# Kernel optimization log

Hardware: AMD Instinct MI355X
Metric: run time of the kernel (lower is better)

Reference implementation:

```python
import jax, jax.numpy as jnp
import numpy as np


def lstm_cell(x, h, c, Wih, Whh, bih, bhh):
    # PyTorch LSTMCell: gates ordered (i, f, g, o)
    gates = x @ Wih.T + h @ Whh.T + bih + bhh
    i, f, g, o = jnp.split(gates, 4, axis=-1)
    c_new = jax.nn.sigmoid(f) * c + jax.nn.sigmoid(i) * jnp.tanh(g)
    h_new = jax.nn.sigmoid(o) * jnp.tanh(c_new)
    return h_new, c_new


def setup_inputs() -> dict:
    key = jax.random.key(0)
    B, S, I, H = 64, 1024, 300, 512
    ks = jax.random.split(key, 9)
    s0 = 1.0 / np.sqrt(H)  # PyTorch LSTMCell default init range

    def u(k, shape):
        return jax.random.uniform(k, shape, jnp.float32, -s0, s0)

    return {
        "input": jax.random.normal(ks[0], (B, S, I), jnp.float32),
        "Wih0": u(ks[1], (4 * H, I)),
        "Whh0": u(ks[2], (4 * H, H)),
        "bih0": u(ks[3], (4 * H,)),
        "bhh0": u(ks[4], (4 * H,)),
        "Wih1": u(ks[5], (4 * H, H)),
        "Whh1": u(ks[6], (4 * H, H)),
        "bih1": u(ks[7], (4 * H,)),
        "bhh1": u(ks[8], (4 * H,)),
    }


def reference(input, Wih0, Whh0, bih0, bhh0, Wih1, Whh1, bih1, bhh1):
    B, S, I = input.shape
    H = Whh0.shape[1]
    h0 = c0 = h1 = c1 = jnp.zeros((B, H), input.dtype)  # self.h0/self.c0 zeros

    def step(carry, x_t):
        h0, c0, h1, c1 = carry
        h0, c0 = lstm_cell(x_t, h0, c0, Wih0, Whh0, bih0, bhh0)
        h1, c1 = lstm_cell(h0, h1, c1, Wih1, Whh1, bih1, bhh1)
        return (h0, c0, h1, c1), (h1, c1)

    xs = jnp.swapaxes(input, 0, 1)  # [S, B, I]
    (h0, c0, h1, c1), (out, c_out) = jax.lax.scan(step, (h0, c0, h1, c1), xs)
    out = jnp.swapaxes(out, 0, 1)      # [B, S, H]
    c_out = jnp.swapaxes(c_out, 0, 1)  # [B, S, H]
    return ((out, c_out), (h1, c1))
```

## Files before the change

### kernel.cpp

```cpp
#include <hip/hip_runtime.h>

#define NB 64
#define NS 1024
#define NI 300
#define NH 512
#define L0WG 32
#define NWG 64

typedef _Float16 f16;
typedef f16 half8 __attribute__((ext_vector_type(8)));
typedef float floatx4 __attribute__((ext_vector_type(4)));
typedef unsigned long long u64;
typedef unsigned u32;
typedef u32 u32x4 __attribute__((ext_vector_type(4)));

__device__ __attribute__((aligned(64))) f16 g_X[NS][NB][320];
__device__ __attribute__((aligned(64))) f16 g_H0[4][NB][NH];
__device__ __attribute__((aligned(64))) f16 g_H1[4][NB][NH];
__device__ u32 g_f0[NS][32];
__device__ u32 g_f1[NS][32];
__device__ u32 g_fI[NWG];

__device__ __forceinline__ float sigm(float x){ return 1.f/(1.f+__expf(-x)); }
__device__ __forceinline__ float tanh_(float x){ return 1.f - 2.f/(__expf(2.f*x)+1.f); }

__device__ __forceinline__ u32 ldc(const u32* p){
  return __hip_atomic_load(p, __ATOMIC_RELAXED, __HIP_MEMORY_SCOPE_AGENT);
}
__device__ __forceinline__ void sig(u32* p, u32 v){
  __hip_atomic_store(p, v, __ATOMIC_RELAXED, __HIP_MEMORY_SCOPE_AGENT);
}

#define STR_(x) #x
#define STR(x) STR_(x)
#define CLOAD16(dst, base, OFF) \
  asm volatile("global_load_dwordx4 %0, %1, off offset:" STR(OFF) " sc1" \
               : "=v"(dst) : "v"(base))
#define CLOADN16(dst, base, OFF) \
  asm volatile("global_load_dwordx4 %0, %1, off offset:" STR(OFF) \
               : "=v"(dst) : "v"(base))
#define CSTORE16(base, val) \
  asm volatile("global_store_dwordx4 %0, %1, off sc1" :: "v"(base), "v"(val))
#define VWAIT(N) do { asm volatile("s_waitcnt vmcnt(" STR(N) ")" ::: "memory"); \
  __builtin_amdgcn_sched_barrier(0); } while(0)
#define MFMA(acc, a, b) acc = __builtin_amdgcn_mfma_f32_16x16x32_f16(a, b, acc, 0, 0, 0)

#define HLOADS(arr, p) do { \
  CLOAD16(arr[0],  p, 0);   CLOAD16(arr[1],  p, 64);  \
  CLOAD16(arr[2],  p, 128); CLOAD16(arr[3],  p, 192); \
  CLOAD16(arr[4],  p, 256); CLOAD16(arr[5],  p, 320); \
  CLOAD16(arr[6],  p, 384); CLOAD16(arr[7],  p, 448); \
  CLOAD16(arr[8],  p, 512); CLOAD16(arr[9],  p, 576); \
  CLOAD16(arr[10], p, 640); CLOAD16(arr[11], p, 704); \
  CLOAD16(arr[12], p, 768); CLOAD16(arr[13], p, 832); \
  CLOAD16(arr[14], p, 896); CLOAD16(arr[15], p, 960); } while(0)

__device__ __forceinline__ void pollA(const u32* pa, const u32* pb, u32 E, int lane){
  const u32* p = nullptr;
  if (lane < 8) p = pa + lane * 4;
  else if (lane < 16 && pb) p = pb + (lane - 8) * 4;
  for (;;){
    bool ok = true;
    if (p){
      u32x4 v;
      asm volatile("global_load_dwordx4 %0, %1, off sc1" : "=v"(v) : "v"(p));
      asm volatile("s_waitcnt vmcnt(0)" ::: "memory");
      ok = ((int)(v[0]-E) >= 0) & ((int)(v[1]-E) >= 0) &
           ((int)(v[2]-E) >= 0) & ((int)(v[3]-E) >= 0);
    }
    if (__all(ok)) return;
    __builtin_amdgcn_s_sleep(1);
  }
}

__global__ void __launch_bounds__(256, 1) lstm_persist(
    const float* __restrict__ xin,
    const float* __restrict__ Wih0, const float* __restrict__ Whh0,
    const float* __restrict__ bih0, const float* __restrict__ bhh0,
    const float* __restrict__ Wih1, const float* __restrict__ Whh1,
    const float* __restrict__ bih1, const float* __restrict__ bhh1,
    float* __restrict__ out)
{
  __shared__ f16   WB[96 * 640];
  __shared__ f16   sh_h[4][16][24];
  __shared__ float sh_o[4][2][16][20];

  const int wg = blockIdx.x, tid = threadIdx.x;
  const int wv = tid >> 6, lane = tid & 63, n15 = lane & 15, g4 = lane >> 4;
  const int kb = g4 * 8;
  const int mrow = wv * 16 + n15;
  const bool isL1 = (wg >= L0WG);
  const int wgi = isL1 ? wg - L0WG : wg;
  const int j0 = wgi * 16;
  const int bb = n15 * 40 + kb;

  const u32 E = ldc(&g_f1[NS - 1][0]) + 1;

  const int jc = j0 + n15;
  float bi, bf, bg, bo;
  float creg[4] = {0.f, 0.f, 0.f, 0.f};

  if (!isL1) {
    bi = bih0[jc] + bhh0[jc];          bf = bih0[NH + jc] + bhh0[NH + jc];
    bg = bih0[2*NH + jc] + bhh0[2*NH + jc]; bo = bih0[3*NH + jc] + bhh0[3*NH + jc];

    {
      const int b = tid >> 2, q = tid & 3;
      for (int r = 0; r < 32; ++r) {
        const int t = wgi * 32 + r;
        const float* xr = xin + ((size_t)b * NS + t) * NI;
        u64* dst = (u64*)&g_X[t][b][0];
        #pragma unroll
        for (int e = 0; e < 20; ++e) {
          const int idx = q * 20 + e;
          u64 v = 0;
          if (idx < 75) {
            const float4 f = *(const float4*)(xr + (idx << 2));
            union { f16 h[4]; u64 u; } pk;
            pk.h[0]=(f16)f.x; pk.h[1]=(f16)f.y; pk.h[2]=(f16)f.z; pk.h[3]=(f16)f.w;
            v = pk.u;
          }
          dst[idx] = v;
        }
      }
    }
    if (tid < 64) {
      half8 z = {};
      CSTORE16(&g_H0[3][tid][j0], z);
      CSTORE16(&g_H0[3][tid][j0 + 8], z);
    }
    for (int idx = tid; idx < 52 * 16; idx += 256) {
      const int u = idx >> 4, n = idx & 15;
      const int gl = 2 + (u >= 26);
      const int ch = (u >= 26) ? u - 26 : u;
      const int grow = gl * NH + j0 + n;
      f16* dst = &WB[u * 640 + n * 40];
      for (int k = 0; k < 32; ++k) {
        const int kk = ch * 32 + k;
        float v;
        if (kk < NI) v = Wih0[(size_t)grow * NI + kk];
        else if (kk < 320) v = 0.f;
        else v = Whh0[(size_t)grow * NH + (kk - 320)];
        dst[k] = (f16)v;
      }
    }
    half8 w_i[26], w_f[26];
    {
      const int gi = j0 + n15, gf = NH + j0 + n15;
      #pragma unroll
      for (int ch = 0; ch < 26; ++ch) {
        union { f16 h[8]; half8 v; } pi, pf;
        #pragma unroll
        for (int jj = 0; jj < 8; ++jj) {
          const int kk = ch * 32 + kb + jj;
          pi.h[jj] = (f16)((kk < NI) ? Wih0[(size_t)gi * NI + kk]
                     : (kk < 320) ? 0.f : Whh0[(size_t)gi * NH + (kk - 320)]);
          pf.h[jj] = (f16)((kk < NI) ? Wih0[(size_t)gf * NI + kk]
                     : (kk < 320) ? 0.f : Whh0[(size_t)gf * NH + (kk - 320)]);
        }
        w_i[ch] = pi.v; w_f[ch] = pf.v;
      }
    }
    VWAIT(0);
    __threadfence();
    __syncthreads();
    if (tid == 0) sig(&g_fI[wg], E);
    if (wv == 0) {
      pollA(&g_fI[0], nullptr, E, lane);
      pollA(&g_fI[32], nullptr, E, lane);
    }
    __syncthreads();

    half8 xa[10];
    {
      const f16* xp = &g_X[0][mrow][0] + kb;
      CLOADN16(xa[0], xp, 0);   CLOADN16(xa[1], xp, 64);
      CLOADN16(xa[2], xp, 128); CLOADN16(xa[3], xp, 192);
      CLOADN16(xa[4], xp, 256); CLOADN16(xa[5], xp, 320);
      CLOADN16(xa[6], xp, 384); CLOADN16(xa[7], xp, 448);
      CLOADN16(xa[8], xp, 512); CLOADN16(xa[9], xp, 576);
    }

    for (int t = 0; t < NS; ++t) {
      if (t > 0) {
        if (wv == 0) pollA(&g_f0[t-1][0], (t >= 4) ? &g_f1[t-4][0] : nullptr, E, lane);
        __syncthreads();
      }
      const f16* hp = &g_H0[(t + 3) & 3][mrow][0] + kb;
      half8 ha[16];
      HLOADS(ha, hp);
      floatx4 ai = {0,0,0,0}, af = {0,0,0,0}, ag = {0,0,0,0}, ao = {0,0,0,0};
      VWAIT(16);
      #pragma unroll
      for (int ci = 0; ci < 10; ++ci) {
        const half8 a = xa[ci];
        MFMA(ai, a, w_i[ci]); MFMA(af, a, w_f[ci]);
        MFMA(ag, a, *(const half8*)&WB[ci * 640 + bb]);
        MFMA(ao, a, *(const half8*)&WB[(26 + ci) * 640 + bb]);
      }
      VWAIT(8);
      #pragma unroll
      for (int ci = 10; ci < 18; ++ci) {
        const half8 a = ha[ci - 10];
        MFMA(ai, a, w_i[ci]); MFMA(af, a, w_f[ci]);
        MFMA(ag, a, *(const half8*)&WB[ci * 640 + bb]);
        MFMA(ao, a, *(const half8*)&WB[(26 + ci) * 640 + bb]);
      }
      VWAIT(0);
      #pragma unroll
      for (int ci = 18; ci < 26; ++ci) {
        const half8 a = ha[ci - 10];
        MFMA(ai, a, w_i[ci]); MFMA(af, a, w_f[ci]);
        MFMA(ag, a, *(const half8*)&WB[ci * 640 + bb]);
        MFMA(ao, a, *(const half8*)&WB[(26 + ci) * 640 + bb]);
      }
      #pragma unroll
      for (int r = 0; r < 4; ++r) {
        const float vi = ai[r] + bi, vf = af[r] + bf;
        const float vg = ag[r] + bg, vo = ao[r] + bo;
        const float cn = sigm(vf) * creg[r] + sigm(vi) * tanh_(vg);
        const float hn = sigm(vo) * tanh_(cn);
        creg[r] = cn;
        sh_h[wv][g4 * 4 + r][n15] = (f16)hn;
      }
      asm volatile("s_waitcnt lgkmcnt(0)" ::: "memory");
      __builtin_amdgcn_sched_barrier(0);
      if (lane < 32) {
        const half8 hv = *(const half8*)&sh_h[wv][lane >> 1][(lane & 1) * 8];
        CSTORE16(&g_H0[t & 3][wv * 16 + (lane >> 1)][j0 + (lane & 1) * 8], hv);
      }
      VWAIT(0);
      __syncthreads();
      if (tid == 0) sig(&g_f0[t][wgi], E);
      if (t + 1 < NS) {
        const f16* xp = &g_X[t + 1][mrow][0] + kb;
        CLOADN16(xa[0], xp, 0);   CLOADN16(xa[1], xp, 64);
        CLOADN16(xa[2], xp, 128); CLOADN16(xa[3], xp, 192);
        CLOADN16(xa[4], xp, 256); CLOADN16(xa[5], xp, 320);
        CLOADN16(xa[6], xp, 384); CLOADN16(xa[7], xp, 448);
        CLOADN16(xa[8], xp, 512); CLOADN16(xa[9], xp, 576);
      }
    }

  } else {
    bi = bih1[jc] + bhh1[jc];          bf = bih1[NH + jc] + bhh1[NH + jc];
    bg = bih1[2*NH + jc] + bhh1[2*NH + jc]; bo = bih1[3*NH + jc] + bhh1[3*NH + jc];

    if (tid < 64) {
      half8 z = {};
      CSTORE16(&g_H1[3][tid][j0], z);
      CSTORE16(&g_H1[3][tid][j0 + 8], z);
    }
    for (int idx = tid; idx < 96 * 16; idx += 256) {
      const int u = idx >> 4, n = idx & 15;
      const int gl = 1 + (u >> 5);
      const int ch = u & 31;
      const int grow = gl * NH + j0 + n;
      f16* dst = &WB[u * 640 + n * 40];
      for (int k = 0; k < 32; ++k) {
        const int kk = ch * 32 + k;
        const float v = (kk < NH) ? Wih1[(size_t)grow * NH + kk]
                                  : Whh1[(size_t)grow * NH + (kk - NH)];
        dst[k] = (f16)v;
      }
    }
    half8 w_i1[32];
    {
      const int gi = j0 + n15;
      #pragma unroll
      for (int ch = 0; ch < 32; ++ch) {
        union { f16 h[8]; half8 v; } pk;
        #pragma unroll
        for (int jj = 0; jj < 8; ++jj) {
          const int kk = ch * 32 + kb + jj;
          pk.h[jj] = (f16)((kk < NH) ? Wih1[(size_t)gi * NH + kk]
                                     : Whh1[(size_t)gi * NH + (kk - NH)]);
        }
        w_i1[ch] = pk.v;
      }
    }
    VWAIT(0);
    __syncthreads();
    if (tid == 0) sig(&g_fI[wg], E);
    if (wv == 0) {
      pollA(&g_fI[0], nullptr, E, lane);
      pollA(&g_fI[32], nullptr, E, lane);
    }
    __syncthreads();

    for (int t = 0; t < NS; ++t) {
      if (wv == 0) pollA(&g_f0[t][0], (t >= 1) ? &g_f1[t-1][0] : nullptr, E, lane);
      __syncthreads();
      const f16* p0 = &g_H0[t & 3][mrow][0] + kb;
      const f16* p1 = &g_H1[(t + 3) & 3][mrow][0] + kb;
      half8 ha[16], hb[16];
      HLOADS(ha, p0);
      HLOADS(hb, p1);
      floatx4 ai = {0,0,0,0}, af = {0,0,0,0}, ag = {0,0,0,0}, ao = {0,0,0,0};
      VWAIT(24);
      #pragma unroll
      for (int ci = 0; ci < 8; ++ci) {
        const half8 a = ha[ci];
        MFMA(ai, a, w_i1[ci]);
        MFMA(af, a, *(const half8*)&WB[ci * 640 + bb]);
        MFMA(ag, a, *(const half8*)&WB[(32 + ci) * 640 + bb]);
        MFMA(ao, a, *(const half8*)&WB[(64 + ci) * 640 + bb]);
      }
      VWAIT(16);
      #pragma unroll
      for (int ci = 8; ci < 16; ++ci) {
        const half8 a = ha[ci];
        MFMA(ai, a, w_i1[ci]);
        MFMA(af, a, *(const half8*)&WB[ci * 640 + bb]);
        MFMA(ag, a, *(const half8*)&WB[(32 + ci) * 640 + bb]);
        MFMA(ao, a, *(const half8*)&WB[(64 + ci) * 640 + bb]);
      }
      VWAIT(8);
      #pragma unroll
      for (int ci = 16; ci < 24; ++ci) {
        const half8 a = hb[ci - 16];
        MFMA(ai, a, w_i1[ci]);
        MFMA(af, a, *(const half8*)&WB[ci * 640 + bb]);
        MFMA(ag, a, *(const half8*)&WB[(32 + ci) * 640 + bb]);
        MFMA(ao, a, *(const half8*)&WB[(64 + ci) * 640 + bb]);
      }
      VWAIT(0);
      #pragma unroll
      for (int ci = 24; ci < 32; ++ci) {
        const half8 a = hb[ci - 16];
        MFMA(ai, a, w_i1[ci]);
        MFMA(af, a, *(const half8*)&WB[ci * 640 + bb]);
        MFMA(ag, a, *(const half8*)&WB[(32 + ci) * 640 + bb]);
        MFMA(ao, a, *(const half8*)&WB[(64 + ci) * 640 + bb]);
      }
      #pragma unroll
      for (int r = 0; r < 4; ++r) {
        const float vi = ai[r] + bi, vf = af[r] + bf;
        const float vg = ag[r] + bg, vo = ao[r] + bo;
        const float cn = sigm(vf) * creg[r] + sigm(vi) * tanh_(vg);
        const float hn = sigm(vo) * tanh_(cn);
        creg[r] = cn;
        sh_h[wv][g4 * 4 + r][n15] = (f16)hn;
        sh_o[wv][0][g4 * 4 + r][n15] = hn;
        sh_o[wv][1][g4 * 4 + r][n15] = cn;
      }
      asm volatile("s_waitcnt lgkmcnt(0)" ::: "memory");
      __builtin_amdgcn_sched_barrier(0);
      if (lane < 32) {
        const half8 hv = *(const half8*)&sh_h[wv][lane >> 1][(lane & 1) * 8];
        CSTORE16(&g_H1[t & 3][wv * 16 + (lane >> 1)][j0 + (lane & 1) * 8], hv);
      }
      {
        const int orow = lane >> 2, of4 = (lane & 3) * 4;
        const int b = wv * 16 + orow;
        const float4 hv4 = *(const float4*)&sh_o[wv][0][orow][of4];
        const float4 cv4 = *(const float4*)&sh_o[wv][1][orow][of4];
        const size_t o1 = ((size_t)b * NS + t) * NH + j0 + of4;
        *(float4*)&out[o1] = hv4;
        *(float4*)&out[(size_t)NB * NS * NH + o1] = cv4;
        if (t == NS - 1) {
          const size_t o2 = 2ull * NB * NS * NH + (size_t)b * NH + j0 + of4;
          *(float4*)&out[o2] = hv4;
          *(float4*)&out[o2 + (size_t)NB * NH] = cv4;
        }
      }
      VWAIT(0);
      __syncthreads();
      if (tid == 0) sig(&g_f1[t][wgi], E);
    }
  }
}

extern "C" void kernel_launch(void* const* d_in, const int* in_sizes, int n_in,
                              void* d_out, int out_size, void* d_ws, size_t ws_size,
                              hipStream_t stream) {
  (void)in_sizes; (void)n_in; (void)d_ws; (void)ws_size; (void)out_size;
  lstm_persist<<<dim3(NWG), dim3(256), 0, stream>>>(
      (const float*)d_in[0],
      (const float*)d_in[1], (const float*)d_in[2],
      (const float*)d_in[3], (const float*)d_in[4],
      (const float*)d_in[5], (const float*)d_in[6],
      (const float*)d_in[7], (const float*)d_in[8],
      (float*)d_out);
}
```

Measured before the change: 9.509 ms.

## Use per-WG monotonic counters for flags and signal before output stores

Replaces the per-timestep flag arrays with one monotonically increasing counter per workgroup in a compact, page-aligned array, so polling always reads the same few cache lines instead of a fresh row every step. Layer-1 workgroups now publish their step-complete flag right after storing h to the exchange buffer, before writing the large fp32 output tensors. This takes the output stores off the critical path of the recurrence, and the stores are drained at the next step's wait instead. It relies on every workgroup reading a consistent base counter at launch, which adds some fragility across repeated launches.

After: 9.556 ms. Within noise of the previous version (+0.5%).

```diff
diff --git a/kernel.cpp b/kernel.cpp
--- a/kernel.cpp
+++ b/kernel.cpp
@@ -17,9 +17,8 @@
 __device__ __attribute__((aligned(64))) f16 g_X[NS][NB][320];
 __device__ __attribute__((aligned(64))) f16 g_H0[4][NB][NH];
 __device__ __attribute__((aligned(64))) f16 g_H1[4][NB][NH];
-__device__ u32 g_f0[NS][32];
-__device__ u32 g_f1[NS][32];
-__device__ u32 g_fI[NWG];
+__device__ __attribute__((aligned(4096))) u32 g_fl0[1024];
+__device__ __attribute__((aligned(4096))) u32 g_fl1[1024];
 
 __device__ __forceinline__ float sigm(float x){ return 1.f/(1.f+__expf(-x)); }
 __device__ __forceinline__ float tanh_(float x){ return 1.f - 2.f/(__expf(2.f*x)+1.f); }
@@ -55,18 +54,19 @@
   CLOAD16(arr[12], p, 768); CLOAD16(arr[13], p, 832); \
   CLOAD16(arr[14], p, 896); CLOAD16(arr[15], p, 960); } while(0)
 
-__device__ __forceinline__ void pollA(const u32* pa, const u32* pb, u32 E, int lane){
-  const u32* p = nullptr;
-  if (lane < 8) p = pa + lane * 4;
-  else if (lane < 16 && pb) p = pb + (lane - 8) * 4;
+__device__ __forceinline__ void pollA2(const u32* pa, u32 ta,
+                                       const u32* pb, u32 tb, int lane){
+  const u32* p = nullptr; u32 tgt = 0;
+  if (lane < 8)       { p = pa + lane * 4;       tgt = ta; }
+  else if (lane < 16) { p = pb + (lane - 8) * 4; tgt = tb; }
   for (;;){
     bool ok = true;
     if (p){
       u32x4 v;
       asm volatile("global_load_dwordx4 %0, %1, off sc1" : "=v"(v) : "v"(p));
       asm volatile("s_waitcnt vmcnt(0)" ::: "memory");
-      ok = ((int)(v[0]-E) >= 0) & ((int)(v[1]-E) >= 0) &
-           ((int)(v[2]-E) >= 0) & ((int)(v[3]-E) >= 0);
+      ok = ((int)(v[0]-tgt) >= 0) & ((int)(v[1]-tgt) >= 0) &
+           ((int)(v[2]-tgt) >= 0) & ((int)(v[3]-tgt) >= 0);
     }
     if (__all(ok)) return;
     __builtin_amdgcn_s_sleep(1);
@@ -89,16 +89,16 @@
   const int wv = tid >> 6, lane = tid & 63, n15 = lane & 15, g4 = lane >> 4;
   const int kb = g4 * 8;
   const int mrow = wv * 16 + n15;
+
   const bool isL1 = (wg >= L0WG);
   const int wgi = isL1 ? wg - L0WG : wg;
   const int j0 = wgi * 16;
   const int bb = n15 * 40 + kb;
-
-  const u32 E = ldc(&g_f1[NS - 1][0]) + 1;
-
   const int jc = j0 + n15;
   float bi, bf, bg, bo;
   float creg[4] = {0.f, 0.f, 0.f, 0.f};
+
+  const u32 base = isL1 ? ldc(&g_fl1[wgi]) : ldc(&g_fl0[wgi]);
 
   if (!isL1) {
     bi = bih0[jc] + bhh0[jc];          bf = bih0[NH + jc] + bhh0[NH + jc];
@@ -164,11 +164,8 @@
     VWAIT(0);
     __threadfence();
     __syncthreads();
-    if (tid == 0) sig(&g_fI[wg], E);
-    if (wv == 0) {
-      pollA(&g_fI[0], nullptr, E, lane);
-      pollA(&g_fI[32], nullptr, E, lane);
-    }
+    if (tid == 0) sig(&g_fl0[wgi], base + 1);
+    if (wv == 0) pollA2(&g_fl0[0], base + 1, &g_fl1[0], base + 1, lane);
     __syncthreads();
 
     half8 xa[10];
@@ -183,7 +180,9 @@
 
     for (int t = 0; t < NS; ++t) {
       if (t > 0) {
-        if (wv == 0) pollA(&g_f0[t-1][0], (t >= 4) ? &g_f1[t-4][0] : nullptr, E, lane);
+        if (wv == 0)
+          pollA2(&g_fl0[0], base + 1 + (u32)t,
+                 &g_fl1[0], (t >= 4) ? base + (u32)t - 2 : base, lane);
         __syncthreads();
       }
       const f16* hp = &g_H0[(t + 3) & 3][mrow][0] + kb;
@@ -231,7 +230,7 @@
       }
       VWAIT(0);
       __syncthreads();
-      if (tid == 0) sig(&g_f0[t][wgi], E);
+      if (tid == 0) sig(&g_fl0[wgi], base + 2 + (u32)t);
       if (t + 1 < NS) {
         const f16* xp = &g_X[t + 1][mrow][0] + kb;
         CLOADN16(xa[0], xp, 0);   CLOADN16(xa[1], xp, 64);
@@ -281,15 +280,17 @@
     }
     VWAIT(0);
     __syncthreads();
-    if (tid == 0) sig(&g_fI[wg], E);
-    if (wv == 0) {
-      pollA(&g_fI[0], nullptr, E, lane);
-      pollA(&g_fI[32], nullptr, E, lane);
-    }
+    if (tid == 0) sig(&g_fl1[wgi], base + 1);
+    if (wv == 0) pollA2(&g_fl0[0], base + 1, &g_fl1[0], base + 1, lane);
     __syncthreads();
 
     for (int t = 0; t < NS; ++t) {
-      if (wv == 0) pollA(&g_f0[t][0], (t >= 1) ? &g_f1[t-1][0] : nullptr, E, lane);
+      if (wv == 0) {
+        pollA2(&g_fl0[0], base + 2 + (u32)t,
+               &g_fl1[0], (t >= 1) ? base + 1 + (u32)t : base, lane);
+      } else {
+        VWAIT(0);
+      }
       __syncthreads();
       const f16* p0 = &g_H0[t & 3][mrow][0] + kb;
       const f16* p1 = &g_H1[(t + 3) & 3][mrow][0] + kb;
@@ -350,6 +351,9 @@
         const half8 hv = *(const half8*)&sh_h[wv][lane >> 1][(lane & 1) * 8];
         CSTORE16(&g_H1[t & 3][wv * 16 + (lane >> 1)][j0 + (lane & 1) * 8], hv);
       }
+      VWAIT(0);
+      __syncthreads();
+      if (tid == 0) sig(&g_fl1[wgi], base + 2 + (u32)t);
       {
         const int orow = lane >> 2, of4 = (lane & 3) * 4;
         const int b = wv * 16 + orow;
@@ -364,9 +368,6 @@
           *(float4*)&out[o2 + (size_t)NB * NH] = cv4;
         }
       }
-      VWAIT(0);
-      __syncthreads();
-      if (tid == 0) sig(&g_f1[t][wgi], E);
     }
   }
 }
```
